# Kernel optimization log

Hardware: AMD Instinct MI355X
Metric: run time of the kernel (lower is better)

## Reference

```python
import jax, jax.numpy as jnp
import numpy as np

KH, KW = 3, 3          # kernel_size
SH, SW = 1, 1          # strides
EM_ITERS = 3           # standard EM routing iteration count
EPS = 1e-9


def to_blocks(x):
    """im2col-style block extraction matching ConvCaps2D._to_blocks.
    x: [B, H, W, ...] -> [B, Ho, Wo, KH, KW, ...] with Ho=(H-KH+1)//SH."""
    Ho = (x.shape[1] - KH + 1) // SH
    Wo = (x.shape[2] - KW + 1) // SW
    rows = []
    for i in range(KH):
        cols = [x[:, i:i + (Ho - 1) * SH + 1:SH, j:j + (Wo - 1) * SW + 1:SW]
                for j in range(KW)]
        rows.append(jnp.stack(cols, axis=3))   # [B,Ho,Wo,KW,...]
    return jnp.stack(rows, axis=3)             # [B,Ho,Wo,KH,KW,...]


def em_routing(votes, a_in, beta_a, beta_u):
    """EM routing (Hinton et al. 2018 matrix capsules).
    votes: [B,Ho,Wo,O,N,D], a_in: [B,Ho,Wo,N], beta_*: [1,1,1,O].
    Returns poses mu [B,Ho,Wo,O,D], activations [B,Ho,Wo,O]."""
    B, Ho, Wo, O, N, D = votes.shape
    R = jnp.full((B, Ho, Wo, O, N), 1.0 / O, dtype=votes.dtype)
    a = a_in[:, :, :, None, :]                                  # [B,Ho,Wo,1,N]
    mu = None
    a_out = None
    for t in range(EM_ITERS):
        inv_temp = 1.0 + t                                      # increasing lambda schedule
        # ---- M-step ----
        r = R * a                                               # [B,Ho,Wo,O,N]
        r_sum = jnp.sum(r, axis=-1, keepdims=True) + EPS        # [B,Ho,Wo,O,1]
        mu = jnp.einsum('bhwon,bhwond->bhwod', r, votes) / r_sum
        diff2 = (votes - mu[:, :, :, :, None, :]) ** 2          # [B,Ho,Wo,O,N,D]
        sigma2 = jnp.einsum('bhwon,bhwond->bhwod', r, diff2) / r_sum + EPS
        cost = jnp.sum((beta_u[..., None] + 0.5 * jnp.log(sigma2)) * r_sum, axis=-1)
        a_out = jax.nn.sigmoid(inv_temp * (beta_a - cost))      # [B,Ho,Wo,O]
        # ---- E-step (skipped after last M-step) ----
        if t < EM_ITERS - 1:
            s2 = sigma2[:, :, :, :, None, :]
            logp = -0.5 * jnp.sum(jnp.log(2.0 * jnp.pi * s2) + diff2 / s2, axis=-1)
            logits = jnp.log(a_out + EPS)[..., None] + logp     # [B,Ho,Wo,O,N]
            R = jax.nn.softmax(logits, axis=3)                  # normalize over output caps
    return mu, a_out


def setup_inputs() -> dict:
    key = jax.random.key(0)
    k1, k2, k3, k4, k5 = jax.random.split(key, 5)
    B, H, W, Cin, d1, d2 = 4, 16, 16, 16, 4, 4
    O = 32
    poses = jax.random.normal(k1, (B, H, W, Cin, d1, d2), dtype=jnp.float32)
    activations = jax.random.uniform(k2, (B, H, W, Cin), dtype=jnp.float32)
    fan_in = KH * KW * Cin * d1 * d2
    kernel = jax.random.normal(k3, (O, KH, KW, Cin, d1, d2), dtype=jnp.float32) * np.sqrt(2.0 / fan_in).astype(np.float32)
    beta_a = jax.random.normal(k4, (1, 1, 1, O), dtype=jnp.float32) * 0.1
    beta_u = jax.random.normal(k5, (1, 1, 1, O), dtype=jnp.float32) * 0.1
    return {"poses": poses, "activations": activations, "kernel": kernel,
            "beta_a": beta_a, "beta_u": beta_u}


def reference(poses, activations, kernel, beta_a, beta_u):
    B, _, _, Cin, d1, d2 = poses.shape
    O = kernel.shape[0]
    pose_blocks = to_blocks(poses)                              # [B,Ho,Wo,KH,KW,Cin,d1,d2]
    # votes = pose @ W per (output channel, kernel offset, input channel)
    votes = jnp.einsum('bhwKLcij,oKLcjl->bhwoKLcil', pose_blocks, kernel)
    Ho, Wo = votes.shape[1], votes.shape[2]
    N = KH * KW * Cin
    votes = votes.reshape(B, Ho, Wo, O, N, d1 * d2)             # [B,Ho,Wo,O,N,D]
    a_blocks = to_blocks(activations).reshape(B, Ho, Wo, N)
    mu, a_out = em_routing(votes, a_blocks, beta_a, beta_u)
    capsule_poses = mu.reshape(B, Ho, Wo, O, d1, d2)
    return capsule_poses, a_out
```

## Files before the change

kernel.cpp:

```cpp
#include <hip/hip_runtime.h>
#include <math.h>

#define NBLK 784
#define O_ 32
#define N_ 144
#define D_ 16
#define PS 20
#define RS 148

__global__ __launch_bounds__(256) void convcaps_em(
    const float* __restrict__ poses,
    const float* __restrict__ acts,
    const float* __restrict__ kern,
    const float* __restrict__ beta_a,
    const float* __restrict__ beta_u,
    float* __restrict__ out)
{
    const int pix = blockIdx.x;
    const int b  = pix / 196;
    const int hw = pix - b * 196;
    const int ho = hw / 14;
    const int wo = hw - ho * 14;

    __shared__ __align__(16) float P[N_ * PS];
    __shared__ float A[N_];
    __shared__ float Rm[O_ * RS];

    const int t = threadIdx.x;

    for (int idx = t; idx < N_ * D_; idx += 256) {
        int n = idx >> 4, d = idx & 15;
        int ki = n / 48, kj = (n >> 4) - ki * 3, c = n & 15;
        P[n * PS + d] = poses[((b * 16 + ho + ki) * 16 + (wo + kj)) * 256 + c * 16 + d];
    }
    if (t < N_) {
        int n = t;
        int ki = n / 48, kj = (n >> 4) - ki * 3, c = n & 15;
        A[n] = acts[((b * 16 + ho + ki) * 16 + (wo + kj)) * 16 + c];
    }
    for (int idx = t; idx < O_ * N_; idx += 256) {
        int oo = idx / N_;
        int nn = idx - oo * N_;
        Rm[oo * RS + nn] = 0.03125f;
    }
    __syncthreads();

    const int o = t >> 3;
    const int s = t & 7;
    const float bu = beta_u[o];
    const float ba = beta_a[o];
    const float* Kbase = kern + (size_t)o * (N_ * D_);

    float a_out = 0.f;
    float mu[16];

    for (int it = 0; it < 3; ++it) {
        float S1[16], S2[16];
#pragma unroll
        for (int d = 0; d < 16; ++d) { S1[d] = 0.f; S2[d] = 0.f; }
        float rs = 0.f;

        for (int k = 0; k < 18; ++k) {
            const int n = s + (k << 3);
            const float r = Rm[o * RS + n] * A[n];
            rs += r;
            float pv[16], kv[16];
            const float4* Pp = (const float4*)(P + n * PS);
            ((float4*)pv)[0] = Pp[0];
            ((float4*)pv)[1] = Pp[1];
            ((float4*)pv)[2] = Pp[2];
            ((float4*)pv)[3] = Pp[3];
            const float4* Kp = (const float4*)(Kbase + n * D_);
            ((float4*)kv)[0] = Kp[0];
            ((float4*)kv)[1] = Kp[1];
            ((float4*)kv)[2] = Kp[2];
            ((float4*)kv)[3] = Kp[3];
#pragma unroll
            for (int i = 0; i < 4; ++i) {
#pragma unroll
                for (int l = 0; l < 4; ++l) {
                    float v = fmaf(pv[i*4+0], kv[0+l],
                              fmaf(pv[i*4+1], kv[4+l],
                              fmaf(pv[i*4+2], kv[8+l],
                                   pv[i*4+3] * kv[12+l])));
                    S1[i*4+l] = fmaf(r, v, S1[i*4+l]);
                    S2[i*4+l] = fmaf(r * v, v, S2[i*4+l]);
                }
            }
        }

#pragma unroll
        for (int m = 1; m < 8; m <<= 1) {
            rs += __shfl_xor(rs, m, 64);
#pragma unroll
            for (int d = 0; d < 16; ++d) {
                S1[d] += __shfl_xor(S1[d], m, 64);
                S2[d] += __shfl_xor(S2[d], m, 64);
            }
        }

        rs += 1e-9f;
        const float inv_rs = 1.0f / rs;
        float sig[16];
#pragma unroll
        for (int d = 0; d < 16; ++d) {
            mu[d] = S1[d] * inv_rs;
            sig[d] = fmaf(-mu[d], mu[d], S2[d] * inv_rs) + 1e-9f;
        }
        float lpart = logf(sig[2*s]) + logf(sig[2*s+1]);
#pragma unroll
        for (int m = 1; m < 8; m <<= 1) lpart += __shfl_xor(lpart, m, 64);
        const float L = lpart;
        const float cost = rs * fmaf(0.5f, L, 16.0f * bu);
        const float x = (float)(it + 1) * (ba - cost);
        a_out = 1.0f / (1.0f + expf(-x));

        if (it < 2) {
            float isig[16];
#pragma unroll
            for (int d = 0; d < 16; ++d) isig[d] = 1.0f / sig[d];
            const float LC = logf(a_out + 1e-9f)
                           - 0.5f * (16.0f * 1.8378770664093453f + L);
            __syncthreads();

            for (int k = 0; k < 18; ++k) {
                const int n = s + (k << 3);
                float pv[16], kv[16];
                const float4* Pp = (const float4*)(P + n * PS);
                ((float4*)pv)[0] = Pp[0];
                ((float4*)pv)[1] = Pp[1];
                ((float4*)pv)[2] = Pp[2];
                ((float4*)pv)[3] = Pp[3];
                const float4* Kp = (const float4*)(Kbase + n * D_);
                ((float4*)kv)[0] = Kp[0];
                ((float4*)kv)[1] = Kp[1];
                ((float4*)kv)[2] = Kp[2];
                ((float4*)kv)[3] = Kp[3];
                float Q = 0.f;
#pragma unroll
                for (int i = 0; i < 4; ++i) {
#pragma unroll
                    for (int l = 0; l < 4; ++l) {
                        float v = fmaf(pv[i*4+0], kv[0+l],
                                  fmaf(pv[i*4+1], kv[4+l],
                                  fmaf(pv[i*4+2], kv[8+l],
                                       pv[i*4+3] * kv[12+l])));
                        const float df = v - mu[i*4+l];
                        Q = fmaf(df * df, isig[i*4+l], Q);
                    }
                }
                Rm[o * RS + n] = fmaf(-0.5f, Q, LC);
            }
            __syncthreads();

            if (t < N_) {
                float v[32];
                float mx = -1e30f;
#pragma unroll
                for (int oo = 0; oo < 32; ++oo) {
                    v[oo] = Rm[oo * RS + t];
                    mx = fmaxf(mx, v[oo]);
                }
                float sm = 0.f;
#pragma unroll
                for (int oo = 0; oo < 32; ++oo) {
                    v[oo] = expf(v[oo] - mx);
                    sm += v[oo];
                }
                const float inv = 1.0f / sm;
#pragma unroll
                for (int oo = 0; oo < 32; ++oo)
                    Rm[oo * RS + t] = v[oo] * inv;
            }
            __syncthreads();
        }
    }

    float2 w2;
    w2.x = mu[2 * s];
    w2.y = mu[2 * s + 1];
    *(float2*)(out + (size_t)pix * 512 + o * 16 + 2 * s) = w2;
    if (s == 0) out[401408 + pix * 32 + o] = a_out;
}

extern "C" void kernel_launch(void* const* d_in, const int* in_sizes, int n_in,
                              void* d_out, int out_size, void* d_ws, size_t ws_size,
                              hipStream_t stream)
{
    const float* poses  = (const float*)d_in[0];
    const float* acts   = (const float*)d_in[1];
    const float* kern   = (const float*)d_in[2];
    const float* beta_a = (const float*)d_in[3];
    const float* beta_u = (const float*)d_in[4];
    float* out = (float*)d_out;
    convcaps_em<<<NBLK, 256, 0, stream>>>(poses, acts, kern, beta_a, beta_u, out);
}
```

Measured before the change: 110.7 us.

## Fold activations into routing weights, use fast math intrinsics, unroll loops

Pre-multiplies the routing matrix by the input activations at init and inside the softmax normalization, which removes a shared-memory load and multiply from the M-step loop. Computes the log-variance sum locally with paired products and fast __logf instead of a shuffle reduction. Swaps expf/logf for __expf/__logf, adds unroll-by-2 on both inner loops, and writes outputs as float4 from one lane per group. Fast intrinsics and log-of-product reduce accuracy slightly, and the extra unrolling may raise register pressure.

After: 102.5 us. 1.08x faster.

```diff
diff --git a/kernel.cpp b/kernel.cpp
--- a/kernel.cpp
+++ b/kernel.cpp
@@ -38,17 +38,18 @@
         int ki = n / 48, kj = (n >> 4) - ki * 3, c = n & 15;
         A[n] = acts[((b * 16 + ho + ki) * 16 + (wo + kj)) * 16 + c];
     }
+    __syncthreads();
     for (int idx = t; idx < O_ * N_; idx += 256) {
         int oo = idx / N_;
         int nn = idx - oo * N_;
-        Rm[oo * RS + nn] = 0.03125f;
+        Rm[oo * RS + nn] = 0.03125f * A[nn];
     }
     __syncthreads();
 
     const int o = t >> 3;
     const int s = t & 7;
-    const float bu = beta_u[o];
-    const float ba = beta_a[o];
+    const float buv = beta_u[o];
+    const float ba  = beta_a[o];
     const float* Kbase = kern + (size_t)o * (N_ * D_);
 
     float a_out = 0.f;
@@ -60,9 +61,10 @@
         for (int d = 0; d < 16; ++d) { S1[d] = 0.f; S2[d] = 0.f; }
         float rs = 0.f;
 
+#pragma unroll 2
         for (int k = 0; k < 18; ++k) {
             const int n = s + (k << 3);
-            const float r = Rm[o * RS + n] * A[n];
+            const float r = Rm[o * RS + n];
             rs += r;
             float pv[16], kv[16];
             const float4* Pp = (const float4*)(P + n * PS);
@@ -107,22 +109,23 @@
             mu[d] = S1[d] * inv_rs;
             sig[d] = fmaf(-mu[d], mu[d], S2[d] * inv_rs) + 1e-9f;
         }
-        float lpart = logf(sig[2*s]) + logf(sig[2*s+1]);
-#pragma unroll
-        for (int m = 1; m < 8; m <<= 1) lpart += __shfl_xor(lpart, m, 64);
-        const float L = lpart;
-        const float cost = rs * fmaf(0.5f, L, 16.0f * bu);
+        const float L = __logf(sig[0]  * sig[1])  + __logf(sig[2]  * sig[3])
+                      + __logf(sig[4]  * sig[5])  + __logf(sig[6]  * sig[7])
+                      + __logf(sig[8]  * sig[9])  + __logf(sig[10] * sig[11])
+                      + __logf(sig[12] * sig[13]) + __logf(sig[14] * sig[15]);
+        const float cost = rs * fmaf(0.5f, L, 16.0f * buv);
         const float x = (float)(it + 1) * (ba - cost);
-        a_out = 1.0f / (1.0f + expf(-x));
+        a_out = 1.0f / (1.0f + __expf(-x));
 
         if (it < 2) {
-            float isig[16];
-#pragma unroll
-            for (int d = 0; d < 16; ++d) isig[d] = 1.0f / sig[d];
-            const float LC = logf(a_out + 1e-9f)
+            float isg[16];
+#pragma unroll
+            for (int d = 0; d < 16; ++d) isg[d] = 1.0f / sig[d];
+            const float LC = __logf(a_out + 1e-9f)
                            - 0.5f * (16.0f * 1.8378770664093453f + L);
             __syncthreads();
 
+#pragma unroll 2
             for (int k = 0; k < 18; ++k) {
                 const int n = s + (k << 3);
                 float pv[16], kv[16];
@@ -146,7 +149,7 @@
                                   fmaf(pv[i*4+2], kv[8+l],
                                        pv[i*4+3] * kv[12+l])));
                         const float df = v - mu[i*4+l];
-                        Q = fmaf(df * df, isig[i*4+l], Q);
+                        Q = fmaf(df * df, isg[i*4+l], Q);
                     }
                 }
                 Rm[o * RS + n] = fmaf(-0.5f, Q, LC);
@@ -164,23 +167,26 @@
                 float sm = 0.f;
 #pragma unroll
                 for (int oo = 0; oo < 32; ++oo) {
-                    v[oo] = expf(v[oo] - mx);
+                    v[oo] = __expf(v[oo] - mx);
                     sm += v[oo];
                 }
-                const float inv = 1.0f / sm;
+                const float sc = A[t] / sm;
 #pragma unroll
                 for (int oo = 0; oo < 32; ++oo)
-                    Rm[oo * RS + t] = v[oo] * inv;
+                    Rm[oo * RS + t] = v[oo] * sc;
             }
             __syncthreads();
         }
     }
 
-    float2 w2;
-    w2.x = mu[2 * s];
-    w2.y = mu[2 * s + 1];
-    *(float2*)(out + (size_t)pix * 512 + o * 16 + 2 * s) = w2;
-    if (s == 0) out[401408 + pix * 32 + o] = a_out;
+    if (s == 0) {
+        float4* ob = (float4*)(out + (size_t)pix * 512 + o * 16);
+        ob[0] = make_float4(mu[0],  mu[1],  mu[2],  mu[3]);
+        ob[1] = make_float4(mu[4],  mu[5],  mu[6],  mu[7]);
+        ob[2] = make_float4(mu[8],  mu[9],  mu[10], mu[11]);
+        ob[3] = make_float4(mu[12], mu[13], mu[14], mu[15]);
+        out[401408 + pix * 32 + o] = a_out;
+    }
 }
 
 extern "C" void kernel_launch(void* const* d_in, const int* in_sizes, int n_in,
```
